# Optimization experiments

Measured on AMD Instinct MI355X. Metric: run time of the kernel, lower is better.

Reference implementation:

```python
import jax, jax.numpy as jnp
import numpy as np

B, T, H, L, O = 128, 1024, 512, 2, 1
SCALE = 0.02  # keep tanh/sigmoid in sane range


def setup_inputs() -> dict:
    key = jax.random.key(0)
    ks = jax.random.split(key, 13)
    return {
        "input": jax.random.normal(ks[0], (B, 8), jnp.float32),
        "hidden": jax.random.normal(ks[1], (L, B, H), jnp.float32) * 0.5,
        "encoder_outputs": jax.random.normal(ks[2], (B, T, H), jnp.float32),
        "attn_w": jax.random.normal(ks[3], (1, (L + 1) * H), jnp.float32) * SCALE,
        "attn_b": jnp.zeros((1,), jnp.float32),
        "comb_w": jax.random.normal(ks[4], (H, H + O), jnp.float32) * SCALE,
        "comb_b": jnp.zeros((H,), jnp.float32),
        "gru_w_ih": jax.random.normal(ks[5], (L, 3 * H, H), jnp.float32) * SCALE,
        "gru_w_hh": jax.random.normal(ks[6], (L, 3 * H, H), jnp.float32) * SCALE,
        "gru_b_ih": jnp.zeros((L, 3 * H), jnp.float32),
        "gru_b_hh": jnp.zeros((L, 3 * H), jnp.float32),
        "out_w": jax.random.normal(ks[7], (O, H), jnp.float32) * SCALE,
        "out_b": jnp.zeros((O,), jnp.float32),
    }


def reference(input, hidden, encoder_outputs, attn_w, attn_b, comb_w, comb_b,
              gru_w_ih, gru_w_hh, gru_b_ih, gru_b_hh, out_w, out_b):
    # input0 = input[:, -1].unsqueeze(1) -> [B, 1]
    input0 = input[:, -1:]
    # hidden [L,B,H] -> hidden_attn [B, L*H]
    hidden_attn = jnp.transpose(hidden, (1, 0, 2)).reshape(hidden.shape[1], -1)
    # Vectorized additive-attention scores (original loops over T):
    # score[b,t] = [hidden_attn_b ; enc_bt] @ attn_w.T + attn_b
    w = attn_w[0]                      # [(L+1)*H]
    w_h, w_e = w[: L * H], w[L * H:]   # [L*H], [H]
    score = (hidden_attn @ w_h)[:, None] + jnp.einsum('bth,h->bt', encoder_outputs, w_e) + attn_b[0]
    attn_weights = jax.nn.softmax(score, axis=1)          # [B, T]
    attn_applied = jnp.einsum('bt,bth->bh', attn_weights, encoder_outputs)  # [B, H]
    # attn_combine + relu (dropout_p = 0 -> identity)
    comb_in = jnp.concatenate([input0, attn_applied], axis=1)  # [B, 1+H]
    x = jax.nn.relu(comb_in @ comb_w.T + comb_b)               # [B, H]
    # single-step multi-layer GRU (PyTorch gate order: r, z, n)
    new_hidden = []
    for l in range(L):
        gx = x @ gru_w_ih[l].T + gru_b_ih[l]             # [B, 3H]
        gh = hidden[l] @ gru_w_hh[l].T + gru_b_hh[l]     # [B, 3H]
        xr, xz, xn = jnp.split(gx, 3, axis=1)
        hr, hz, hn = jnp.split(gh, 3, axis=1)
        r = jax.nn.sigmoid(xr + hr)
        z = jax.nn.sigmoid(xz + hz)
        n = jnp.tanh(xn + r * hn)
        h_new = (1.0 - z) * n + z * hidden[l]
        new_hidden.append(h_new)
        x = h_new
    hidden_out = jnp.stack(new_hidden, axis=0)           # [L, B, H]
    output = x @ out_w.T + out_b                         # [B, O]
    return output, hidden_out, attn_weights[:, None, :]
```

## Files before the change

### kernel.cpp

```cpp
#include <hip/hip_runtime.h>
#include <math.h>

#define B 128
#define T 1024
#define H 512
#define L 2
#define G3H 1536
#define CH 32
#define KS 2

typedef __attribute__((ext_vector_type(8))) short bf16x8;
typedef __attribute__((ext_vector_type(4))) float f32x4;

__global__ __launch_bounds__(256)
void attn_fused_kernel(const float* __restrict__ enc,
                       const float* __restrict__ attn_w,
                       float* __restrict__ score_out,
                       float* __restrict__ part,
                       float* __restrict__ stats) {
    int c = blockIdx.x, b = blockIdx.y;
    int tid = threadIdx.x, lane = tid & 63, wave = tid >> 6;
    int chunk = c * 4 + wave;
    int t0 = chunk * 32;

    const float4 we0 = *(const float4*)(attn_w + L * H + lane * 8);
    const float4 we1 = *(const float4*)(attn_w + L * H + lane * 8 + 4);

    const float* rp = enc + ((size_t)b * T + t0) * H + lane * 8;

    float l_run = 0.0f;
    float acc[8] = {0, 0, 0, 0, 0, 0, 0, 0};
    float my_s = 0.0f;

#pragma unroll 4
    for (int r = 0; r < 32; r++) {
        float4 e0 = *(const float4*)(rp + (size_t)r * H);
        float4 e1 = *(const float4*)(rp + (size_t)r * H + 4);
        float d = e0.x * we0.x + e0.y * we0.y + e0.z * we0.z + e0.w * we0.w
                + e1.x * we1.x + e1.y * we1.y + e1.z * we1.z + e1.w * we1.w;
#pragma unroll
        for (int off = 32; off; off >>= 1) d += __shfl_xor(d, off);
        if (lane == r) my_s = d;
        float w = __expf(d);
        l_run += w;
        acc[0] += w * e0.x; acc[1] += w * e0.y;
        acc[2] += w * e0.z; acc[3] += w * e0.w;
        acc[4] += w * e1.x; acc[5] += w * e1.y;
        acc[6] += w * e1.z; acc[7] += w * e1.w;
    }
    if (lane < 32) score_out[b * T + t0 + lane] = my_s;
    float* pp = part + ((size_t)chunk * B + b) * H + lane * 8;
    float4 o0 = {acc[0], acc[1], acc[2], acc[3]};
    float4 o1 = {acc[4], acc[5], acc[6], acc[7]};
    *(float4*)pp       = o0;
    *(float4*)(pp + 4) = o1;
    if (lane == 0) stats[chunk * B + b] = l_run;
}

__global__ void comb_kernel(const float* __restrict__ part,
                            const float* __restrict__ stats,
                            const float* __restrict__ score,
                            const float* __restrict__ input,
                            const float* __restrict__ comb_w,
                            const float* __restrict__ comb_b,
                            float* __restrict__ x_out,
                            float* __restrict__ attnw) {
    int q = blockIdx.x, b = blockIdx.y, tid = threadIdx.x;
    int lane = tid & 63, wave = tid >> 6;
    __shared__ float at[H];

    float l_fin = 0.0f;
#pragma unroll
    for (int k = 0; k < CH; k++) l_fin += stats[k * B + b];
    float inv = 1.0f / l_fin;
    float ax = 0.0f, ay = 0.0f;
#pragma unroll 8
    for (int k = 0; k < CH; k++) {
        ax += part[((size_t)k * B + b) * H + tid];
        ay += part[((size_t)k * B + b) * H + tid + 256];
    }
    at[tid]       = ax * inv;
    at[tid + 256] = ay * inv;
    if (q == 0) {
        float4 sv = *(const float4*)(score + b * T + tid * 4);
        float4 ov = { __expf(sv.x) * inv, __expf(sv.y) * inv,
                      __expf(sv.z) * inv, __expf(sv.w) * inv };
        *(float4*)(attnw + b * T + tid * 4) = ov;
    }
    __syncthreads();

    float in0 = input[b * 8 + 7];
    float areg[8];
#pragma unroll
    for (int j = 0; j < 8; j++) areg[j] = at[j * 64 + lane];
    for (int r = 0; r < 32; r++) {
        int h = q * 128 + wave * 32 + r;
        const float* wr = comb_w + (size_t)h * (H + 1);
        float d = 0.0f;
#pragma unroll
        for (int j = 0; j < 8; j++) d += areg[j] * wr[1 + j * 64 + lane];
#pragma unroll
        for (int off = 32; off; off >>= 1) d += __shfl_xor(d, off);
        if (lane == 0)
            x_out[(size_t)b * H + h] = fmaxf(0.0f, d + in0 * wr[0] + comb_b[h]);
    }
}

__device__ inline short f2bf(float f) {
    union { float f; unsigned u; } v; v.f = f;
    unsigned r = v.u + 0x7fffu + ((v.u >> 16) & 1u);
    return (short)(r >> 16);
}

__device__ inline bf16x8 load_frag(const float* __restrict__ p) {
    float4 a = *(const float4*)p;
    float4 b = *(const float4*)(p + 4);
    bf16x8 r;
    r[0] = f2bf(a.x); r[1] = f2bf(a.y); r[2] = f2bf(a.z); r[3] = f2bf(a.w);
    r[4] = f2bf(b.x); r[5] = f2bf(b.y); r[6] = f2bf(b.z); r[7] = f2bf(b.w);
    return r;
}

__global__ __launch_bounds__(64)
void gemm_mfma_kernel(const float* __restrict__ A0,
                      const float* __restrict__ A1,
                      const float* __restrict__ W0,
                      const float* __restrict__ W1,
                      float* __restrict__ C0,
                      float* __restrict__ C1) {
    int job = blockIdx.x;
    int sel = job & 1, ks = (job >> 1) & (KS - 1), mh = (job >> 2) & 1, nt = job >> 3;
    const float* A = sel ? A1 : A0;
    const float* W = sel ? W1 : W0;
    float* Cp = (sel ? C1 : C0) + (size_t)ks * B * G3H;
    int lane = threadIdx.x;
    int row16 = lane & 15, quad = lane >> 4;
    int n0 = nt * 16, m0 = mh * 64;
    int kb = ks * (H / KS);
    const float* Wp = W + (size_t)(n0 + row16) * H + kb + quad * 8;
    const float* Ap = A + (size_t)(m0 + row16) * H + kb + quad * 8;
    f32x4 acc0 = {0.f, 0.f, 0.f, 0.f}, acc1 = acc0, acc2 = acc0, acc3 = acc0;
#pragma unroll 2
    for (int k = 0; k < H / KS; k += 32) {
        bf16x8 bw = load_frag(Wp + k);
        bf16x8 a0 = load_frag(Ap + k);
        bf16x8 a1 = load_frag(Ap + 16 * H + k);
        bf16x8 a2 = load_frag(Ap + 32 * H + k);
        bf16x8 a3 = load_frag(Ap + 48 * H + k);
        acc0 = __builtin_amdgcn_mfma_f32_16x16x32_bf16(a0, bw, acc0, 0, 0, 0);
        acc1 = __builtin_amdgcn_mfma_f32_16x16x32_bf16(a1, bw, acc1, 0, 0, 0);
        acc2 = __builtin_amdgcn_mfma_f32_16x16x32_bf16(a2, bw, acc2, 0, 0, 0);
        acc3 = __builtin_amdgcn_mfma_f32_16x16x32_bf16(a3, bw, acc3, 0, 0, 0);
    }
    int col = n0 + row16;
    int rb = m0 + quad * 4;
#pragma unroll
    for (int reg = 0; reg < 4; reg++) {
        Cp[(size_t)(rb + reg) * G3H + col]      = acc0[reg];
        Cp[(size_t)(rb + 16 + reg) * G3H + col] = acc1[reg];
        Cp[(size_t)(rb + 32 + reg) * G3H + col] = acc2[reg];
        Cp[(size_t)(rb + 48 + reg) * G3H + col] = acc3[reg];
    }
}

__global__ __launch_bounds__(512)
void gates_kernel(const float* __restrict__ gx,
                  const float* __restrict__ gh,
                  const float* __restrict__ b_ih,
                  const float* __restrict__ b_hh,
                  const float* __restrict__ hprev,
                  float* __restrict__ hid_out,
                  float* __restrict__ x_out,
                  const float* __restrict__ out_w,
                  const float* __restrict__ out_b,
                  float* __restrict__ out,
                  int last) {
    int b = blockIdx.x, h = threadIdx.x;
    int lane = h & 63, wave = h >> 6;
    size_t gb = (size_t)b * G3H;
    float xr = b_ih[h], xz = b_ih[H + h], xn = b_ih[2 * H + h];
    float hr = b_hh[h], hz = b_hh[H + h], hn = b_hh[2 * H + h];
#pragma unroll
    for (int k = 0; k < KS; k++) {
        size_t o = (size_t)k * B * G3H + gb;
        xr += gx[o + h];         xz += gx[o + H + h];     xn += gx[o + 2 * H + h];
        hr += gh[o + h];         hz += gh[o + H + h];     hn += gh[o + 2 * H + h];
    }
    float hp = hprev[(size_t)b * H + h];
    float r = 1.0f / (1.0f + expf(-(xr + hr)));
    float z = 1.0f / (1.0f + expf(-(xz + hz)));
    float n = tanhf(xn + r * hn);
    float hnew = (1.0f - z) * n + z * hp;
    hid_out[(size_t)b * H + h] = hnew;
    x_out[(size_t)b * H + h] = hnew;
    if (last) {
        __shared__ float red[8];
        float d = hnew * out_w[h];
#pragma unroll
        for (int off = 32; off; off >>= 1) d += __shfl_xor(d, off);
        if (lane == 0) red[wave] = d;
        __syncthreads();
        if (h == 0) {
            float s = out_b[0];
#pragma unroll
            for (int i = 0; i < 8; i++) s += red[i];
            out[b] = s;
        }
    }
}

extern "C" void kernel_launch(void* const* d_in, const int* in_sizes, int n_in,
                              void* d_out, int out_size, void* d_ws, size_t ws_size,
                              hipStream_t stream) {
    const float* input  = (const float*)d_in[0];
    const float* hidden = (const float*)d_in[1];
    const float* enc    = (const float*)d_in[2];
    const float* attn_w = (const float*)d_in[3];
    const float* comb_w = (const float*)d_in[5];
    const float* comb_b = (const float*)d_in[6];
    const float* w_ih   = (const float*)d_in[7];
    const float* w_hh   = (const float*)d_in[8];
    const float* b_ih   = (const float*)d_in[9];
    const float* b_hh   = (const float*)d_in[10];
    const float* out_w  = (const float*)d_in[11];
    const float* out_b  = (const float*)d_in[12];

    float* out = (float*)d_out;
    float* hid_out = out + B;
    float* attnw   = out + B + L * B * H;

    float* ws      = (float*)d_ws;
    float* score   = ws;
    float* part    = score + B * T;
    float* stats   = part + (size_t)CH * B * H;
    float* x       = stats + CH * B;
    float* gx      = x + B * H;
    float* gh      = gx + KS * B * G3H;

    attn_fused_kernel<<<dim3(8, B), 256, 0, stream>>>(enc, attn_w, score, part, stats);
    comb_kernel<<<dim3(4, B), 256, 0, stream>>>(part, stats, score, input,
                                                comb_w, comb_b, x, attnw);

    for (int l = 0; l < L; l++) {
        const float* hl = hidden + (size_t)l * B * H;
        gemm_mfma_kernel<<<dim3((G3H / 16) * 2 * KS * 2), 64, 0, stream>>>(
            x, hl,
            w_ih + (size_t)l * G3H * H, w_hh + (size_t)l * G3H * H,
            gx, gh);
        gates_kernel<<<dim3(B), 512, 0, stream>>>(
            gx, gh, b_ih + l * G3H, b_hh + l * G3H, hl,
            hid_out + (size_t)l * B * H, x,
            out_w, out_b, out, l == L - 1);
    }
}
```

Before: 446.8 us.

## Fuse attention with hidden GEMM and collapse combine plus GRU into one tail kernel

The hidden-state GEMMs for both GRU layers do not depend on attention, so they now run as extra MFMA blocks inside the attention launch. Attention combine, both layers' input GEMVs, the gates and the output projection are merged into one per-batch kernel of 1024 threads that keeps intermediates in shared memory. This cuts the launch count from six to two and removes the global round trips for x and gx. In exchange, the input-weight products become FP32 wave-level dot products: each of the 128 batch blocks streams the full w_ih and comb_w matrices, which adds heavy L2 traffic and serial latency per block.

```diff
diff --git a/kernel.cpp b/kernel.cpp
--- a/kernel.cpp
+++ b/kernel.cpp
@@ -12,14 +12,72 @@
 typedef __attribute__((ext_vector_type(8))) short bf16x8;
 typedef __attribute__((ext_vector_type(4))) float f32x4;
 
+__device__ inline short f2bf(float f) {
+    union { float f; unsigned u; } v; v.f = f;
+    unsigned r = v.u + 0x7fffu + ((v.u >> 16) & 1u);
+    return (short)(r >> 16);
+}
+
+__device__ inline bf16x8 load_frag(const float* p) {
+    float4 a = *(const float4*)p;
+    float4 b = *(const float4*)(p + 4);
+    bf16x8 r;
+    r[0] = f2bf(a.x); r[1] = f2bf(a.y); r[2] = f2bf(a.z); r[3] = f2bf(a.w);
+    r[4] = f2bf(b.x); r[5] = f2bf(b.y); r[6] = f2bf(b.z); r[7] = f2bf(b.w);
+    return r;
+}
+
 __global__ __launch_bounds__(256)
-void attn_fused_kernel(const float* __restrict__ enc,
-                       const float* __restrict__ attn_w,
-                       float* __restrict__ score_out,
-                       float* __restrict__ part,
-                       float* __restrict__ stats) {
-    int c = blockIdx.x, b = blockIdx.y;
+void attn_gh_kernel(const float* __restrict__ enc,
+                    const float* __restrict__ attn_w,
+                    const float* __restrict__ hidden,
+                    const float* __restrict__ w_hh,
+                    float* __restrict__ score_out,
+                    float* __restrict__ part,
+                    float* __restrict__ stats,
+                    float* __restrict__ gh) {
+    int bid = blockIdx.x;
     int tid = threadIdx.x, lane = tid & 63, wave = tid >> 6;
+
+    if (bid >= 1024) {
+        int job = (bid - 1024) * 4 + wave;
+        int l  = job >= 384;
+        int jj = job - l * 384;
+        int ks = jj & 1, mh = (jj >> 1) & 1, nt = jj >> 2;
+        const float* A = hidden + (size_t)l * B * H;
+        const float* W = w_hh + (size_t)l * G3H * H;
+        float* Cp = gh + ((size_t)l * KS + ks) * B * G3H;
+        int row16 = lane & 15, quad = lane >> 4;
+        int n0 = nt * 16, m0 = mh * 64;
+        int kb = ks * (H / KS);
+        const float* Wp = W + (size_t)(n0 + row16) * H + kb + quad * 8;
+        const float* Ap = A + (size_t)(m0 + row16) * H + kb + quad * 8;
+        f32x4 acc0 = {0.f, 0.f, 0.f, 0.f}, acc1 = acc0, acc2 = acc0, acc3 = acc0;
+#pragma unroll 2
+        for (int k = 0; k < H / KS; k += 32) {
+            bf16x8 bw = load_frag(Wp + k);
+            bf16x8 a0 = load_frag(Ap + k);
+            bf16x8 a1 = load_frag(Ap + 16 * H + k);
+            bf16x8 a2 = load_frag(Ap + 32 * H + k);
+            bf16x8 a3 = load_frag(Ap + 48 * H + k);
+            acc0 = __builtin_amdgcn_mfma_f32_16x16x32_bf16(a0, bw, acc0, 0, 0, 0);
+            acc1 = __builtin_amdgcn_mfma_f32_16x16x32_bf16(a1, bw, acc1, 0, 0, 0);
+            acc2 = __builtin_amdgcn_mfma_f32_16x16x32_bf16(a2, bw, acc2, 0, 0, 0);
+            acc3 = __builtin_amdgcn_mfma_f32_16x16x32_bf16(a3, bw, acc3, 0, 0, 0);
+        }
+        int col = n0 + row16;
+        int rb = m0 + quad * 4;
+#pragma unroll
+        for (int reg = 0; reg < 4; reg++) {
+            Cp[(size_t)(rb + reg) * G3H + col]      = acc0[reg];
+            Cp[(size_t)(rb + 16 + reg) * G3H + col] = acc1[reg];
+            Cp[(size_t)(rb + 32 + reg) * G3H + col] = acc2[reg];
+            Cp[(size_t)(rb + 48 + reg) * G3H + col] = acc3[reg];
+        }
+        return;
+    }
+
+    int c = bid >> 7, b = bid & 127;
     int chunk = c * 4 + wave;
     int t0 = chunk * 32;
 
@@ -57,155 +115,130 @@
     if (lane == 0) stats[chunk * B + b] = l_run;
 }
 
-__global__ void comb_kernel(const float* __restrict__ part,
-                            const float* __restrict__ stats,
-                            const float* __restrict__ score,
-                            const float* __restrict__ input,
-                            const float* __restrict__ comb_w,
-                            const float* __restrict__ comb_b,
-                            float* __restrict__ x_out,
-                            float* __restrict__ attnw) {
-    int q = blockIdx.x, b = blockIdx.y, tid = threadIdx.x;
-    int lane = tid & 63, wave = tid >> 6;
-    __shared__ float at[H];
-
-    float l_fin = 0.0f;
-#pragma unroll
-    for (int k = 0; k < CH; k++) l_fin += stats[k * B + b];
-    float inv = 1.0f / l_fin;
-    float ax = 0.0f, ay = 0.0f;
-#pragma unroll 8
-    for (int k = 0; k < CH; k++) {
-        ax += part[((size_t)k * B + b) * H + tid];
-        ay += part[((size_t)k * B + b) * H + tid + 256];
-    }
-    at[tid]       = ax * inv;
-    at[tid + 256] = ay * inv;
-    if (q == 0) {
-        float4 sv = *(const float4*)(score + b * T + tid * 4);
-        float4 ov = { __expf(sv.x) * inv, __expf(sv.y) * inv,
-                      __expf(sv.z) * inv, __expf(sv.w) * inv };
-        *(float4*)(attnw + b * T + tid * 4) = ov;
+__global__ __launch_bounds__(1024)
+void tail_kernel(const float* __restrict__ part,
+                 const float* __restrict__ stats,
+                 const float* __restrict__ score,
+                 const float* __restrict__ input,
+                 const float* __restrict__ comb_w,
+                 const float* __restrict__ comb_b,
+                 const float* __restrict__ w_ih,
+                 const float* __restrict__ b_ih,
+                 const float* __restrict__ b_hh,
+                 const float* __restrict__ hidden,
+                 const float* __restrict__ gh,
+                 const float* __restrict__ out_w,
+                 const float* __restrict__ out_b,
+                 float* __restrict__ out,
+                 float* __restrict__ hid_out,
+                 float* __restrict__ attnw) {
+    int b = blockIdx.x, tid = threadIdx.x, lane = tid & 63, wave = tid >> 6;
+    __shared__ float sm_a0[H], sm_a1[H];
+    __shared__ float sm_x[H];
+    __shared__ float sm_g[G3H];
+    __shared__ float sm_h[H];
+    __shared__ float sm_red[8];
+    __shared__ float sm_inv;
+
+    if (tid < 64) {
+        float v = (tid < 32) ? stats[tid * B + b] : 0.0f;
+#pragma unroll
+        for (int off = 32; off; off >>= 1) v += __shfl_xor(v, off);
+        if (tid == 0) sm_inv = 1.0f / v;
+    }
+    {
+        int h = tid & (H - 1), half = tid >> 9;
+        float s = 0.0f;
+#pragma unroll
+        for (int k = 0; k < 16; k++)
+            s += part[(size_t)((half * 16 + k) * B + b) * H + h];
+        (half ? sm_a1 : sm_a0)[h] = s;
     }
     __syncthreads();
-
-    float in0 = input[b * 8 + 7];
-    float areg[8];
-#pragma unroll
-    for (int j = 0; j < 8; j++) areg[j] = at[j * 64 + lane];
-    for (int r = 0; r < 32; r++) {
-        int h = q * 128 + wave * 32 + r;
-        const float* wr = comb_w + (size_t)h * (H + 1);
-        float d = 0.0f;
-#pragma unroll
-        for (int j = 0; j < 8; j++) d += areg[j] * wr[1 + j * 64 + lane];
-#pragma unroll
-        for (int off = 32; off; off >>= 1) d += __shfl_xor(d, off);
-        if (lane == 0)
-            x_out[(size_t)b * H + h] = fmaxf(0.0f, d + in0 * wr[0] + comb_b[h]);
-    }
-}
-
-__device__ inline short f2bf(float f) {
-    union { float f; unsigned u; } v; v.f = f;
-    unsigned r = v.u + 0x7fffu + ((v.u >> 16) & 1u);
-    return (short)(r >> 16);
-}
-
-__device__ inline bf16x8 load_frag(const float* __restrict__ p) {
-    float4 a = *(const float4*)p;
-    float4 b = *(const float4*)(p + 4);
-    bf16x8 r;
-    r[0] = f2bf(a.x); r[1] = f2bf(a.y); r[2] = f2bf(a.z); r[3] = f2bf(a.w);
-    r[4] = f2bf(b.x); r[5] = f2bf(b.y); r[6] = f2bf(b.z); r[7] = f2bf(b.w);
-    return r;
-}
-
-__global__ __launch_bounds__(64)
-void gemm_mfma_kernel(const float* __restrict__ A0,
-                      const float* __restrict__ A1,
-                      const float* __restrict__ W0,
-                      const float* __restrict__ W1,
-                      float* __restrict__ C0,
-                      float* __restrict__ C1) {
-    int job = blockIdx.x;
-    int sel = job & 1, ks = (job >> 1) & (KS - 1), mh = (job >> 2) & 1, nt = job >> 3;
-    const float* A = sel ? A1 : A0;
-    const float* W = sel ? W1 : W0;
-    float* Cp = (sel ? C1 : C0) + (size_t)ks * B * G3H;
-    int lane = threadIdx.x;
-    int row16 = lane & 15, quad = lane >> 4;
-    int n0 = nt * 16, m0 = mh * 64;
-    int kb = ks * (H / KS);
-    const float* Wp = W + (size_t)(n0 + row16) * H + kb + quad * 8;
-    const float* Ap = A + (size_t)(m0 + row16) * H + kb + quad * 8;
-    f32x4 acc0 = {0.f, 0.f, 0.f, 0.f}, acc1 = acc0, acc2 = acc0, acc3 = acc0;
-#pragma unroll 2
-    for (int k = 0; k < H / KS; k += 32) {
-        bf16x8 bw = load_frag(Wp + k);
-        bf16x8 a0 = load_frag(Ap + k);
-        bf16x8 a1 = load_frag(Ap + 16 * H + k);
-        bf16x8 a2 = load_frag(Ap + 32 * H + k);
-        bf16x8 a3 = load_frag(Ap + 48 * H + k);
-        acc0 = __builtin_amdgcn_mfma_f32_16x16x32_bf16(a0, bw, acc0, 0, 0, 0);
-        acc1 = __builtin_amdgcn_mfma_f32_16x16x32_bf16(a1, bw, acc1, 0, 0, 0);
-        acc2 = __builtin_amdgcn_mfma_f32_16x16x32_bf16(a2, bw, acc2, 0, 0, 0);
-        acc3 = __builtin_amdgcn_mfma_f32_16x16x32_bf16(a3, bw, acc3, 0, 0, 0);
-    }
-    int col = n0 + row16;
-    int rb = m0 + quad * 4;
-#pragma unroll
-    for (int reg = 0; reg < 4; reg++) {
-        Cp[(size_t)(rb + reg) * G3H + col]      = acc0[reg];
-        Cp[(size_t)(rb + 16 + reg) * G3H + col] = acc1[reg];
-        Cp[(size_t)(rb + 32 + reg) * G3H + col] = acc2[reg];
-        Cp[(size_t)(rb + 48 + reg) * G3H + col] = acc3[reg];
-    }
-}
-
-__global__ __launch_bounds__(512)
-void gates_kernel(const float* __restrict__ gx,
-                  const float* __restrict__ gh,
-                  const float* __restrict__ b_ih,
-                  const float* __restrict__ b_hh,
-                  const float* __restrict__ hprev,
-                  float* __restrict__ hid_out,
-                  float* __restrict__ x_out,
-                  const float* __restrict__ out_w,
-                  const float* __restrict__ out_b,
-                  float* __restrict__ out,
-                  int last) {
-    int b = blockIdx.x, h = threadIdx.x;
-    int lane = h & 63, wave = h >> 6;
-    size_t gb = (size_t)b * G3H;
-    float xr = b_ih[h], xz = b_ih[H + h], xn = b_ih[2 * H + h];
-    float hr = b_hh[h], hz = b_hh[H + h], hn = b_hh[2 * H + h];
-#pragma unroll
-    for (int k = 0; k < KS; k++) {
-        size_t o = (size_t)k * B * G3H + gb;
-        xr += gx[o + h];         xz += gx[o + H + h];     xn += gx[o + 2 * H + h];
-        hr += gh[o + h];         hz += gh[o + H + h];     hn += gh[o + 2 * H + h];
-    }
-    float hp = hprev[(size_t)b * H + h];
-    float r = 1.0f / (1.0f + expf(-(xr + hr)));
-    float z = 1.0f / (1.0f + expf(-(xz + hz)));
-    float n = tanhf(xn + r * hn);
-    float hnew = (1.0f - z) * n + z * hp;
-    hid_out[(size_t)b * H + h] = hnew;
-    x_out[(size_t)b * H + h] = hnew;
-    if (last) {
-        __shared__ float red[8];
-        float d = hnew * out_w[h];
-#pragma unroll
-        for (int off = 32; off; off >>= 1) d += __shfl_xor(d, off);
-        if (lane == 0) red[wave] = d;
+    float inv = sm_inv;
+
+    attnw[(size_t)b * T + tid] = __expf(score[(size_t)b * T + tid]) * inv;
+
+    {
+        float areg[8];
+#pragma unroll
+        for (int j = 0; j < 8; j++) {
+            int k = j * 64 + lane;
+            areg[j] = (sm_a0[k] + sm_a1[k]) * inv;
+        }
+        float in0 = input[b * 8 + 7];
+        for (int cc = 0; cc < H / 16; cc++) {
+            int h = wave * (H / 16) + cc;
+            const float* wr = comb_w + (size_t)h * (H + 1);
+            float d = 0.0f;
+#pragma unroll
+            for (int j = 0; j < 8; j++) d += areg[j] * wr[1 + j * 64 + lane];
+#pragma unroll
+            for (int off = 32; off; off >>= 1) d += __shfl_xor(d, off);
+            if (lane == 0)
+                sm_x[h] = fmaxf(0.0f, d + in0 * wr[0] + comb_b[h]);
+        }
+    }
+    __syncthreads();
+
+    for (int l = 0; l < L; l++) {
+        {
+            const float* act = l ? sm_h : sm_x;
+            float hreg[8];
+#pragma unroll
+            for (int j = 0; j < 8; j++) hreg[j] = act[lane * 8 + j];
+            const float* wl = w_ih + (size_t)l * G3H * H;
+            for (int cc = 0; cc < G3H / 16; cc++) {
+                int col = wave * (G3H / 16) + cc;
+                const float* wr = wl + (size_t)col * H + lane * 8;
+                float4 w0 = *(const float4*)wr;
+                float4 w1 = *(const float4*)(wr + 4);
+                float d = hreg[0] * w0.x + hreg[1] * w0.y
+                        + hreg[2] * w0.z + hreg[3] * w0.w
+                        + hreg[4] * w1.x + hreg[5] * w1.y
+                        + hreg[6] * w1.z + hreg[7] * w1.w;
+#pragma unroll
+                for (int off = 32; off; off >>= 1) d += __shfl_xor(d, off);
+                if (lane == 0) sm_g[col] = d;
+            }
+        }
         __syncthreads();
-        if (h == 0) {
-            float s = out_b[0];
-#pragma unroll
-            for (int i = 0; i < 8; i++) s += red[i];
-            out[b] = s;
-        }
+
+        float hnew = 0.0f;
+        if (tid < H) {
+            int h = tid;
+            float xr = sm_g[h]         + b_ih[l * G3H + h];
+            float xz = sm_g[H + h]     + b_ih[l * G3H + H + h];
+            float xn = sm_g[2 * H + h] + b_ih[l * G3H + 2 * H + h];
+            float hr = b_hh[l * G3H + h];
+            float hz = b_hh[l * G3H + H + h];
+            float hn = b_hh[l * G3H + 2 * H + h];
+#pragma unroll
+            for (int k = 0; k < KS; k++) {
+                size_t o = ((size_t)l * KS + k) * B * G3H + (size_t)b * G3H;
+                hr += gh[o + h]; hz += gh[o + H + h]; hn += gh[o + 2 * H + h];
+            }
+            float hp = hidden[(size_t)l * B * H + (size_t)b * H + h];
+            float r = 1.0f / (1.0f + __expf(-(xr + hr)));
+            float z = 1.0f / (1.0f + __expf(-(xz + hz)));
+            float n = tanhf(xn + r * hn);
+            hnew = (1.0f - z) * n + z * hp;
+            hid_out[(size_t)l * B * H + (size_t)b * H + h] = hnew;
+            sm_h[h] = hnew;
+            if (l == L - 1) {
+                float d = hnew * out_w[h];
+#pragma unroll
+                for (int off = 32; off; off >>= 1) d += __shfl_xor(d, off);
+                if (lane == 0) sm_red[wave] = d;
+            }
+        }
+        __syncthreads();
+    }
+    if (tid == 0) {
+        float s = out_b[0];
+#pragma unroll
+        for (int i = 0; i < 8; i++) s += sm_red[i];
+        out[b] = s;
     }
 }
 
@@ -233,23 +266,11 @@
     float* score   = ws;
     float* part    = score + B * T;
     float* stats   = part + (size_t)CH * B * H;
-    float* x       = stats + CH * B;
-    float* gx      = x + B * H;
-    float* gh      = gx + KS * B * G3H;
-
-    attn_fused_kernel<<<dim3(8, B), 256, 0, stream>>>(enc, attn_w, score, part, stats);
-    comb_kernel<<<dim3(4, B), 256, 0, stream>>>(part, stats, score, input,
-                                                comb_w, comb_b, x, attnw);
-
-    for (int l = 0; l < L; l++) {
-        const float* hl = hidden + (size_t)l * B * H;
-        gemm_mfma_kernel<<<dim3((G3H / 16) * 2 * KS * 2), 64, 0, stream>>>(
-            x, hl,
-            w_ih + (size_t)l * G3H * H, w_hh + (size_t)l * G3H * H,
-            gx, gh);
-        gates_kernel<<<dim3(B), 512, 0, stream>>>(
-            gx, gh, b_ih + l * G3H, b_hh + l * G3H, hl,
-            hid_out + (size_t)l * B * H, x,
-            out_w, out_b, out, l == L - 1);
-    }
-}
+    float* gh      = stats + CH * B;
+
+    attn_gh_kernel<<<dim3(1024 + 192), 256, 0, stream>>>(
+        enc, attn_w, hidden, w_hh, score, part, stats, gh);
+    tail_kernel<<<dim3(B), 1024, 0, stream>>>(
+        part, stats, score, input, comb_w, comb_b, w_ih, b_ih, b_hh,
+        hidden, gh, out_w, out_b, out, hid_out, attnw);
+}
```

New measurement: 562.0 us. 25.8% more time.

## Fold hidden-state GEMMs into attention kernel and fuse input GEMM with GRU gates

Applied to the files above, without the earlier changes.

The hidden-to-hidden GRU GEMMs for both layers depend only on inputs, so they are computed up front as extra blocks of the attention kernel. Each layer's input GEMM is fused with the gate nonlinearity and hidden update in one MFMA kernel, and the final output projection is accumulated with atomics. This cuts the launch count from six to four, removes the gx round trip through memory, and overlaps the gh work with the bandwidth-bound attention pass. In exchange, the fused GEMM runs only 256 single-wave blocks with the full K loop, and the output now relies on atomic accumulation order.

```diff
diff --git a/kernel.cpp b/kernel.cpp
--- a/kernel.cpp
+++ b/kernel.cpp
@@ -12,14 +12,75 @@
 typedef __attribute__((ext_vector_type(8))) short bf16x8;
 typedef __attribute__((ext_vector_type(4))) float f32x4;
 
+__device__ inline short f2bf(float f) {
+    union { float f; unsigned u; } v; v.f = f;
+    unsigned r = v.u + 0x7fffu + ((v.u >> 16) & 1u);
+    return (short)(r >> 16);
+}
+
+__device__ inline bf16x8 load_frag(const float* p) {
+    float4 a = *(const float4*)p;
+    float4 b = *(const float4*)(p + 4);
+    bf16x8 r;
+    r[0] = f2bf(a.x); r[1] = f2bf(a.y); r[2] = f2bf(a.z); r[3] = f2bf(a.w);
+    r[4] = f2bf(b.x); r[5] = f2bf(b.y); r[6] = f2bf(b.z); r[7] = f2bf(b.w);
+    return r;
+}
+
 __global__ __launch_bounds__(256)
-void attn_fused_kernel(const float* __restrict__ enc,
-                       const float* __restrict__ attn_w,
-                       float* __restrict__ score_out,
-                       float* __restrict__ part,
-                       float* __restrict__ stats) {
-    int c = blockIdx.x, b = blockIdx.y;
+void attn_gh_kernel(const float* __restrict__ enc,
+                    const float* __restrict__ attn_w,
+                    const float* __restrict__ hidden,
+                    const float* __restrict__ w_hh,
+                    const float* __restrict__ out_b,
+                    float* __restrict__ out,
+                    float* __restrict__ score_out,
+                    float* __restrict__ part,
+                    float* __restrict__ stats,
+                    float* __restrict__ gh) {
+    int bid = blockIdx.x;
     int tid = threadIdx.x, lane = tid & 63, wave = tid >> 6;
+
+    if (bid >= 1024) {
+        if (bid == 1024 && tid < B) out[tid] = out_b[0];
+        int job = (bid - 1024) * 4 + wave;
+        int l  = job >= 384;
+        int jj = job - l * 384;
+        int ks = jj & 1, mh = (jj >> 1) & 1, nt = jj >> 2;
+        const float* A = hidden + (size_t)l * B * H;
+        const float* W = w_hh + (size_t)l * G3H * H;
+        float* Cp = gh + ((size_t)l * KS + ks) * B * G3H;
+        int row16 = lane & 15, quad = lane >> 4;
+        int n0 = nt * 16, m0 = mh * 64;
+        int kb = ks * (H / KS);
+        const float* Wp = W + (size_t)(n0 + row16) * H + kb + quad * 8;
+        const float* Ap = A + (size_t)(m0 + row16) * H + kb + quad * 8;
+        f32x4 acc0 = {0.f, 0.f, 0.f, 0.f}, acc1 = acc0, acc2 = acc0, acc3 = acc0;
+#pragma unroll 2
+        for (int k = 0; k < H / KS; k += 32) {
+            bf16x8 bw = load_frag(Wp + k);
+            bf16x8 a0 = load_frag(Ap + k);
+            bf16x8 a1 = load_frag(Ap + 16 * H + k);
+            bf16x8 a2 = load_frag(Ap + 32 * H + k);
+            bf16x8 a3 = load_frag(Ap + 48 * H + k);
+            acc0 = __builtin_amdgcn_mfma_f32_16x16x32_bf16(a0, bw, acc0, 0, 0, 0);
+            acc1 = __builtin_amdgcn_mfma_f32_16x16x32_bf16(a1, bw, acc1, 0, 0, 0);
+            acc2 = __builtin_amdgcn_mfma_f32_16x16x32_bf16(a2, bw, acc2, 0, 0, 0);
+            acc3 = __builtin_amdgcn_mfma_f32_16x16x32_bf16(a3, bw, acc3, 0, 0, 0);
+        }
+        int col = n0 + row16;
+        int rb = m0 + quad * 4;
+#pragma unroll
+        for (int reg = 0; reg < 4; reg++) {
+            Cp[(size_t)(rb + reg) * G3H + col]      = acc0[reg];
+            Cp[(size_t)(rb + 16 + reg) * G3H + col] = acc1[reg];
+            Cp[(size_t)(rb + 32 + reg) * G3H + col] = acc2[reg];
+            Cp[(size_t)(rb + 48 + reg) * G3H + col] = acc3[reg];
+        }
+        return;
+    }
+
+    int c = bid >> 7, b = bid & 127;
     int chunk = c * 4 + wave;
     int t0 = chunk * 32;
 
@@ -106,105 +167,59 @@
     }
 }
 
-__device__ inline short f2bf(float f) {
-    union { float f; unsigned u; } v; v.f = f;
-    unsigned r = v.u + 0x7fffu + ((v.u >> 16) & 1u);
-    return (short)(r >> 16);
-}
-
-__device__ inline bf16x8 load_frag(const float* __restrict__ p) {
-    float4 a = *(const float4*)p;
-    float4 b = *(const float4*)(p + 4);
-    bf16x8 r;
-    r[0] = f2bf(a.x); r[1] = f2bf(a.y); r[2] = f2bf(a.z); r[3] = f2bf(a.w);
-    r[4] = f2bf(b.x); r[5] = f2bf(b.y); r[6] = f2bf(b.z); r[7] = f2bf(b.w);
-    return r;
-}
-
 __global__ __launch_bounds__(64)
-void gemm_mfma_kernel(const float* __restrict__ A0,
-                      const float* __restrict__ A1,
-                      const float* __restrict__ W0,
-                      const float* __restrict__ W1,
-                      float* __restrict__ C0,
-                      float* __restrict__ C1) {
+void gemmgates_kernel(const float* __restrict__ act,
+                      const float* __restrict__ w,
+                      const float* __restrict__ bih,
+                      const float* __restrict__ bhh,
+                      const float* __restrict__ ghl,
+                      const float* __restrict__ hprev,
+                      float* __restrict__ hout,
+                      const float* __restrict__ out_w,
+                      float* __restrict__ out,
+                      int last) {
     int job = blockIdx.x;
-    int sel = job & 1, ks = (job >> 1) & (KS - 1), mh = (job >> 2) & 1, nt = job >> 3;
-    const float* A = sel ? A1 : A0;
-    const float* W = sel ? W1 : W0;
-    float* Cp = (sel ? C1 : C0) + (size_t)ks * B * G3H;
+    int bt = job >> 5, ht = job & 31;
     int lane = threadIdx.x;
     int row16 = lane & 15, quad = lane >> 4;
-    int n0 = nt * 16, m0 = mh * 64;
-    int kb = ks * (H / KS);
-    const float* Wp = W + (size_t)(n0 + row16) * H + kb + quad * 8;
-    const float* Ap = A + (size_t)(m0 + row16) * H + kb + quad * 8;
-    f32x4 acc0 = {0.f, 0.f, 0.f, 0.f}, acc1 = acc0, acc2 = acc0, acc3 = acc0;
-#pragma unroll 2
-    for (int k = 0; k < H / KS; k += 32) {
-        bf16x8 bw = load_frag(Wp + k);
-        bf16x8 a0 = load_frag(Ap + k);
-        bf16x8 a1 = load_frag(Ap + 16 * H + k);
-        bf16x8 a2 = load_frag(Ap + 32 * H + k);
-        bf16x8 a3 = load_frag(Ap + 48 * H + k);
-        acc0 = __builtin_amdgcn_mfma_f32_16x16x32_bf16(a0, bw, acc0, 0, 0, 0);
-        acc1 = __builtin_amdgcn_mfma_f32_16x16x32_bf16(a1, bw, acc1, 0, 0, 0);
-        acc2 = __builtin_amdgcn_mfma_f32_16x16x32_bf16(a2, bw, acc2, 0, 0, 0);
-        acc3 = __builtin_amdgcn_mfma_f32_16x16x32_bf16(a3, bw, acc3, 0, 0, 0);
-    }
-    int col = n0 + row16;
-    int rb = m0 + quad * 4;
+    int b0 = bt * 16, h0 = ht * 16;
+    const float* Ap = act + (size_t)(b0 + row16) * H + quad * 8;
+    const float* Wp = w + (size_t)(h0 + row16) * H + quad * 8;
+    f32x4 ar = {0.f, 0.f, 0.f, 0.f}, az = ar, an = ar;
+#pragma unroll 4
+    for (int k = 0; k < H; k += 32) {
+        bf16x8 a  = load_frag(Ap + k);
+        bf16x8 w0 = load_frag(Wp + k);
+        bf16x8 w1 = load_frag(Wp + (size_t)H * H + k);
+        bf16x8 w2 = load_frag(Wp + (size_t)2 * H * H + k);
+        ar = __builtin_amdgcn_mfma_f32_16x16x32_bf16(a, w0, ar, 0, 0, 0);
+        az = __builtin_amdgcn_mfma_f32_16x16x32_bf16(a, w1, az, 0, 0, 0);
+        an = __builtin_amdgcn_mfma_f32_16x16x32_bf16(a, w2, an, 0, 0, 0);
+    }
+    int h = h0 + row16;
+    float bir = bih[h], biz = bih[H + h], bin = bih[2 * H + h];
+    float bhr = bhh[h], bhz = bhh[H + h], bhn = bhh[2 * H + h];
+    float ow = last ? out_w[h] : 0.0f;
 #pragma unroll
     for (int reg = 0; reg < 4; reg++) {
-        Cp[(size_t)(rb + reg) * G3H + col]      = acc0[reg];
-        Cp[(size_t)(rb + 16 + reg) * G3H + col] = acc1[reg];
-        Cp[(size_t)(rb + 32 + reg) * G3H + col] = acc2[reg];
-        Cp[(size_t)(rb + 48 + reg) * G3H + col] = acc3[reg];
-    }
-}
-
-__global__ __launch_bounds__(512)
-void gates_kernel(const float* __restrict__ gx,
-                  const float* __restrict__ gh,
-                  const float* __restrict__ b_ih,
-                  const float* __restrict__ b_hh,
-                  const float* __restrict__ hprev,
-                  float* __restrict__ hid_out,
-                  float* __restrict__ x_out,
-                  const float* __restrict__ out_w,
-                  const float* __restrict__ out_b,
-                  float* __restrict__ out,
-                  int last) {
-    int b = blockIdx.x, h = threadIdx.x;
-    int lane = h & 63, wave = h >> 6;
-    size_t gb = (size_t)b * G3H;
-    float xr = b_ih[h], xz = b_ih[H + h], xn = b_ih[2 * H + h];
-    float hr = b_hh[h], hz = b_hh[H + h], hn = b_hh[2 * H + h];
-#pragma unroll
-    for (int k = 0; k < KS; k++) {
-        size_t o = (size_t)k * B * G3H + gb;
-        xr += gx[o + h];         xz += gx[o + H + h];     xn += gx[o + 2 * H + h];
-        hr += gh[o + h];         hz += gh[o + H + h];     hn += gh[o + 2 * H + h];
-    }
-    float hp = hprev[(size_t)b * H + h];
-    float r = 1.0f / (1.0f + expf(-(xr + hr)));
-    float z = 1.0f / (1.0f + expf(-(xz + hz)));
-    float n = tanhf(xn + r * hn);
-    float hnew = (1.0f - z) * n + z * hp;
-    hid_out[(size_t)b * H + h] = hnew;
-    x_out[(size_t)b * H + h] = hnew;
-    if (last) {
-        __shared__ float red[8];
-        float d = hnew * out_w[h];
-#pragma unroll
-        for (int off = 32; off; off >>= 1) d += __shfl_xor(d, off);
-        if (lane == 0) red[wave] = d;
-        __syncthreads();
-        if (h == 0) {
-            float s = out_b[0];
-#pragma unroll
-            for (int i = 0; i < 8; i++) s += red[i];
-            out[b] = s;
+        int b = b0 + quad * 4 + reg;
+        const float* g0 = ghl + (size_t)b * G3H;
+        const float* g1 = ghl + (size_t)B * G3H + (size_t)b * G3H;
+        float hr = bhr + g0[h]         + g1[h];
+        float hz = bhz + g0[H + h]     + g1[H + h];
+        float hn = bhn + g0[2 * H + h] + g1[2 * H + h];
+        float xr = ar[reg] + bir, xz = az[reg] + biz, xn = an[reg] + bin;
+        float r = 1.0f / (1.0f + __expf(-(xr + hr)));
+        float z = 1.0f / (1.0f + __expf(-(xz + hz)));
+        float n = tanhf(xn + r * hn);
+        float hp = hprev[(size_t)b * H + h];
+        float hnew = (1.0f - z) * n + z * hp;
+        hout[(size_t)b * H + h] = hnew;
+        if (last) {
+            float p = hnew * ow;
+#pragma unroll
+            for (int off = 1; off < 16; off <<= 1) p += __shfl_xor(p, off);
+            if (row16 == 0) atomicAdd(&out[b], p);
         }
     }
 }
@@ -233,23 +248,17 @@
     float* score   = ws;
     float* part    = score + B * T;
     float* stats   = part + (size_t)CH * B * H;
-    float* x       = stats + CH * B;
-    float* gx      = x + B * H;
-    float* gh      = gx + KS * B * G3H;
-
-    attn_fused_kernel<<<dim3(8, B), 256, 0, stream>>>(enc, attn_w, score, part, stats);
+    float* gh      = stats + CH * B;
+    float* x       = gh + (size_t)L * KS * B * G3H;
+
+    attn_gh_kernel<<<dim3(1024 + 192), 256, 0, stream>>>(
+        enc, attn_w, hidden, w_hh, out_b, out, score, part, stats, gh);
     comb_kernel<<<dim3(4, B), 256, 0, stream>>>(part, stats, score, input,
                                                 comb_w, comb_b, x, attnw);
-
-    for (int l = 0; l < L; l++) {
-        const float* hl = hidden + (size_t)l * B * H;
-        gemm_mfma_kernel<<<dim3((G3H / 16) * 2 * KS * 2), 64, 0, stream>>>(
-            x, hl,
-            w_ih + (size_t)l * G3H * H, w_hh + (size_t)l * G3H * H,
-            gx, gh);
-        gates_kernel<<<dim3(B), 512, 0, stream>>>(
-            gx, gh, b_ih + l * G3H, b_hh + l * G3H, hl,
-            hid_out + (size_t)l * B * H, x,
-            out_w, out_b, out, l == L - 1);
-    }
-}
+    gemmgates_kernel<<<dim3(256), 64, 0, stream>>>(
+        x, w_ih, b_ih, b_hh, gh, hidden, hid_out, out_w, out, 0);
+    gemmgates_kernel<<<dim3(256), 64, 0, stream>>>(
+        hid_out, w_ih + (size_t)G3H * H, b_ih + G3H, b_hh + G3H,
+        gh + (size_t)KS * B * G3H, hidden + (size_t)B * H,
+        hid_out + (size_t)B * H, out_w, out, 1);
+}
```

Measured after the change: 463.2 us. 3.7% more time.
